# Kernel tuning notes

Measured on AMD Instinct MI355X. Metric: run time of the kernel, lower is better.

The kernel has to match this reference:

```python
import jax, jax.numpy as jnp
import numpy as np

VOCAB = 40
EPS = 1e-8

def setup_inputs() -> dict:
    key = jax.random.key(0)
    B, L = 262144, 64
    x = jax.random.randint(key, (B, L), 0, VOCAB, dtype=jnp.int64 if jax.config.jax_enable_x64 else jnp.int32)
    return {"x": x}

def reference(x) -> jnp.ndarray:
    # Batched histogram: counts[b, v] = #occurrences of v in row b.
    B, L = x.shape
    counts = jnp.zeros((B, VOCAB), dtype=jnp.float32)
    rows = jnp.arange(B, dtype=x.dtype)[:, None]              # [B, 1]
    counts = counts.at[rows, x].add(1.0)                       # [B, VOCAB]
    probs = counts / (counts.sum(axis=1, keepdims=True) + EPS)
    entropy = -jnp.sum(probs * jnp.log(probs + EPS), axis=1)   # [B]
    return entropy[:, None]                                    # [B, 1]
```

## Files before the change

### kernel.cpp

```cpp
#include <hip/hip_runtime.h>
#include <math.h>


#define NVOCAB 40
#define EPSF 1e-8f

constexpr int BLOCK = 256;
constexpr int WPB = BLOCK / 64;

__global__ __launch_bounds__(BLOCK) void entropy_hist_kernel(
    const int* __restrict__ x, float* __restrict__ out, int total_groups) {
  __shared__ float G[64];
  __shared__ int hist[WPB][4][NVOCAB];

  const int tid  = threadIdx.x;
  const int lane = tid & 63;
  const int wv   = tid >> 6;
  const int row  = lane >> 4;
  const int sub  = lane & 15;

  if (tid < 64) {
    float c1 = (float)(tid + 1);
    float F1 = c1 * logf(c1 * (1.0f / 64.0f) + EPSF);
    float F0 = 0.0f;
    if (tid > 0) {
      float c0 = (float)tid;
      F0 = c0 * logf(c0 * (1.0f / 64.0f) + EPSF);
    }
    G[tid] = F1 - F0;
  }
  for (int i = tid; i < WPB * 4 * NVOCAB; i += BLOCK) (&hist[0][0][0])[i] = 0;
  __syncthreads();

  int* __restrict__ h = hist[wv][row];

  const int wave_gid    = blockIdx.x * WPB + wv;
  const int total_waves = gridDim.x * WPB;
  const int4* __restrict__ x4 = (const int4*)x;

  int g = wave_gid;
  int4 cur = make_int4(0, 0, 0, 0);
  if (g < total_groups) cur = x4[(long)g * 64 + lane];

  while (g < total_groups) {
    const int gn = g + total_waves;
    int4 nxt = make_int4(0, 0, 0, 0);
    if (gn < total_groups) nxt = x4[(long)gn * 64 + lane];

    int o0 = atomicAdd(&h[cur.x], 1);
    int o1 = atomicAdd(&h[cur.y], 1);
    int o2 = atomicAdd(&h[cur.z], 1);
    int o3 = atomicAdd(&h[cur.w], 1);

    float s = G[o0] + G[o1] + G[o2] + G[o3];

    h[cur.x] = 0; h[cur.y] = 0; h[cur.z] = 0; h[cur.w] = 0;

    s += __shfl_xor(s, 1, 16);
    s += __shfl_xor(s, 2, 16);
    s += __shfl_xor(s, 4, 16);
    s += __shfl_xor(s, 8, 16);

    if (sub == 0) out[g * 4 + row] = s * (-1.0f / 64.0f);

    cur = nxt;
    g = gn;
  }
}

extern "C" void kernel_launch(void* const* d_in, const int* in_sizes, int n_in,
                              void* d_out, int out_size, void* d_ws, size_t ws_size,
                              hipStream_t stream) {
  const int* x = (const int*)d_in[0];
  float* out = (float*)d_out;

  const int n = in_sizes[0];
  const int total_groups = n / 256;

  int blocks = 2048;
  const int max_blocks = (total_groups + WPB - 1) / WPB;
  if (blocks > max_blocks) blocks = max_blocks;
  if (blocks < 1) blocks = 1;

  entropy_hist_kernel<<<blocks, BLOCK, 0, stream>>>(x, out, total_groups);
}
```

Baseline: 91.16 us.

## Assign one row per lane with packed byte histograms in private LDS slots

Replaces the 16-lanes-per-row scheme with one row per lane. Each wave loads 64 rows and packs four tokens per int into a transposed LDS tile. Each lane then builds a private histogram of packed 8-bit counters (4 bins per word) and computes the entropy directly with fast log. This removes the shared-counter atomic contention, the G-table lookups and the cross-lane shuffle reductions. In exchange it uses more LDS per block and loses the software prefetch of the next group. It also relies on token values and counts fitting in 8 bits.

```diff
diff --git a/kernel.cpp b/kernel.cpp
--- a/kernel.cpp
+++ b/kernel.cpp
@@ -3,68 +3,96 @@
 
 
 #define NVOCAB 40
-#define EPSF 1e-8f
 
 constexpr int BLOCK = 256;
-constexpr int WPB = BLOCK / 64;
+constexpr int WPB = 4;
+constexpr int TSTRIDE = 20;
+constexpr int HSTRIDE = 12;
 
-__global__ __launch_bounds__(BLOCK) void entropy_hist_kernel(
-    const int* __restrict__ x, float* __restrict__ out, int total_groups) {
-  __shared__ float G[64];
-  __shared__ int hist[WPB][4][NVOCAB];
+__global__ __launch_bounds__(BLOCK) void entropy_rowlane_kernel(
+    const int* __restrict__ x, float* __restrict__ out, int nbatch) {
+  __shared__ int tile[WPB * 64 * TSTRIDE];
+  __shared__ int hist[WPB * 64 * HSTRIDE];
 
-  const int tid  = threadIdx.x;
-  const int lane = tid & 63;
-  const int wv   = tid >> 6;
-  const int row  = lane >> 4;
-  const int sub  = lane & 15;
+  const int tid = threadIdx.x;
+  const int l   = tid & 63;
+  const int wv  = tid >> 6;
 
-  if (tid < 64) {
-    float c1 = (float)(tid + 1);
-    float F1 = c1 * logf(c1 * (1.0f / 64.0f) + EPSF);
-    float F0 = 0.0f;
-    if (tid > 0) {
-      float c0 = (float)tid;
-      F0 = c0 * logf(c0 * (1.0f / 64.0f) + EPSF);
+  int* const tbase = &tile[wv * 64 * TSTRIDE];
+  int* const hbase = &hist[(wv * 64 + l) * HSTRIDE];
+
+  const int4 z = make_int4(0, 0, 0, 0);
+  ((int4*)hbase)[0] = z;
+  ((int4*)hbase)[1] = z;
+  ((int4*)hbase)[2] = z;
+
+  const int4* const x4 = (const int4*)x;
+
+  int batch = blockIdx.x * WPB + wv;
+  const int batch_step = gridDim.x * WPB;
+
+  for (; batch < nbatch; batch += batch_step) {
+    const long base4 = (long)batch * 1024;
+
+    int4 va[8], vb[8];
+#pragma unroll
+    for (int t = 0; t < 8; ++t) va[t] = x4[base4 + t * 64 + l];
+#pragma unroll
+    for (int t = 0; t < 8; ++t) vb[t] = x4[base4 + (t + 8) * 64 + l];
+
+    const int wrow = l >> 4;
+    const int wcol = l & 15;
+#pragma unroll
+    for (int t = 0; t < 8; ++t) {
+      int p = va[t].x | (va[t].y << 8) | (va[t].z << 16) | (va[t].w << 24);
+      tbase[(4 * t + wrow) * TSTRIDE + wcol] = p;
     }
-    G[tid] = F1 - F0;
-  }
-  for (int i = tid; i < WPB * 4 * NVOCAB; i += BLOCK) (&hist[0][0][0])[i] = 0;
-  __syncthreads();
+#pragma unroll
+    for (int t = 0; t < 8; ++t) {
+      int p = vb[t].x | (vb[t].y << 8) | (vb[t].z << 16) | (vb[t].w << 24);
+      tbase[(4 * (t + 8) + wrow) * TSTRIDE + wcol] = p;
+    }
 
-  int* __restrict__ h = hist[wv][row];
+    __builtin_amdgcn_wave_barrier();
 
-  const int wave_gid    = blockIdx.x * WPB + wv;
-  const int total_waves = gridDim.x * WPB;
-  const int4* __restrict__ x4 = (const int4*)x;
+    const int4* const rbase = (const int4*)(tbase + l * TSTRIDE);
+    int4 r0 = rbase[0], r1 = rbase[1], r2 = rbase[2], r3 = rbase[3];
+    int rw[16] = {r0.x, r0.y, r0.z, r0.w, r1.x, r1.y, r1.z, r1.w,
+                  r2.x, r2.y, r2.z, r2.w, r3.x, r3.y, r3.z, r3.w};
 
-  int g = wave_gid;
-  int4 cur = make_int4(0, 0, 0, 0);
-  if (g < total_groups) cur = x4[(long)g * 64 + lane];
+#pragma unroll
+    for (int i = 0; i < 16; ++i) {
+      unsigned w = (unsigned)rw[i];
+#pragma unroll
+      for (int b = 0; b < 4; ++b) {
+        unsigned v = (w >> (8 * b)) & 0xFFu;
+        atomicAdd((unsigned*)&hbase[v >> 2], 1u << ((v << 3) & 24u));
+      }
+    }
 
-  while (g < total_groups) {
-    const int gn = g + total_waves;
-    int4 nxt = make_int4(0, 0, 0, 0);
-    if (gn < total_groups) nxt = x4[(long)gn * 64 + lane];
+    __builtin_amdgcn_wave_barrier();
 
-    int o0 = atomicAdd(&h[cur.x], 1);
-    int o1 = atomicAdd(&h[cur.y], 1);
-    int o2 = atomicAdd(&h[cur.z], 1);
-    int o3 = atomicAdd(&h[cur.w], 1);
+    int4 h0 = ((int4*)hbase)[0];
+    int4 h1 = ((int4*)hbase)[1];
+    int4 h2 = ((int4*)hbase)[2];
+    ((int4*)hbase)[0] = z;
+    ((int4*)hbase)[1] = z;
+    ((int4*)hbase)[2] = z;
 
-    float s = G[o0] + G[o1] + G[o2] + G[o3];
+    int hw[10] = {h0.x, h0.y, h0.z, h0.w, h1.x, h1.y, h1.z, h1.w, h2.x, h2.y};
+    float s = 0.0f;
+#pragma unroll
+    for (int i = 0; i < 10; ++i) {
+      unsigned w = (unsigned)hw[i];
+#pragma unroll
+      for (int b = 0; b < 4; ++b) {
+        float c = (float)((w >> (8 * b)) & 0xFFu);
+        float p = c * 0.015625f;
+        s += p * __logf(p + 1e-8f);
+      }
+    }
 
-    h[cur.x] = 0; h[cur.y] = 0; h[cur.z] = 0; h[cur.w] = 0;
-
-    s += __shfl_xor(s, 1, 16);
-    s += __shfl_xor(s, 2, 16);
-    s += __shfl_xor(s, 4, 16);
-    s += __shfl_xor(s, 8, 16);
-
-    if (sub == 0) out[g * 4 + row] = s * (-1.0f / 64.0f);
-
-    cur = nxt;
-    g = gn;
+    out[(long)batch * 64 + l] = -s;
   }
 }
 
@@ -75,12 +103,11 @@
   float* out = (float*)d_out;
 
   const int n = in_sizes[0];
-  const int total_groups = n / 256;
+  const int nbatch = n / 4096;
 
-  int blocks = 2048;
-  const int max_blocks = (total_groups + WPB - 1) / WPB;
-  if (blocks > max_blocks) blocks = max_blocks;
+  int blocks = (nbatch + WPB - 1) / WPB;
+  if (blocks > 2048) blocks = 2048;
   if (blocks < 1) blocks = 1;
 
-  entropy_hist_kernel<<<blocks, BLOCK, 0, stream>>>(x, out, total_groups);
+  entropy_rowlane_kernel<<<blocks, BLOCK, 0, stream>>>(x, out, nbatch);
 }
```

New measurement: 91.54 us. No clear change (+0.4%).
